# Kernel tuning notes

Hardware: AMD Instinct MI355X
Metric: run time of the kernel (lower is better)

The kernel has to match this reference:

```python
import jax, jax.numpy as jnp
import numpy as np

N_NODES = 50000


def graph_conv(src, dst, x, W, b, n_nodes):
    """DGL GraphConv, norm='both': D_out^{-1/2} A D_in^{-1/2} x W + b.
    src/dst: [E] edge endpoints (message flows src -> dst).
    """
    ones = jnp.ones(src.shape[0], dtype=x.dtype)
    deg_out = jnp.clip(jax.ops.segment_sum(ones, src, num_segments=n_nodes), 1.0)
    deg_in = jnp.clip(jax.ops.segment_sum(ones, dst, num_segments=n_nodes), 1.0)
    h = x * jax.lax.rsqrt(deg_out)[:, None]          # src-side normalization
    msgs = h[src]                                     # [E, F] gather (irregular)
    agg = jax.ops.segment_sum(msgs, dst, num_segments=n_nodes)  # SpMM scatter-add
    agg = agg * jax.lax.rsqrt(deg_in)[:, None]        # dst-side normalization
    return agg @ W + b


def setup_inputs() -> dict:
    key = jax.random.key(0)
    ks = jax.random.split(key, 9)
    E = 600000
    in_f, hid, emb = 128, 64, 32
    features = jax.random.normal(ks[0], (N_NODES, in_f), dtype=jnp.float32)
    src = jax.random.randint(ks[1], (E,), 0, N_NODES)
    dst = jax.random.randint(ks[2], (E,), 0, N_NODES)

    def glorot(k, fan_in, fan_out):
        lim = np.sqrt(6.0 / (fan_in + fan_out)).astype(np.float32)
        return jax.random.uniform(k, (fan_in, fan_out), jnp.float32, -lim, lim)

    return {
        "features": features, "src": src, "dst": dst,
        "W1": glorot(ks[3], in_f, hid), "b1": jnp.zeros((hid,), jnp.float32),
        "W2": glorot(ks[4], hid, emb), "b2": jnp.zeros((emb,), jnp.float32),
        "W3": glorot(ks[5], emb, in_f), "b3": jnp.zeros((in_f,), jnp.float32),
    }


def reference(features, src, dst, W1, b1, W2, b2, W3, b3):
    h = jax.nn.relu(graph_conv(src, dst, features, W1, b1, N_NODES))
    z = graph_conv(src, dst, h, W2, b2, N_NODES)
    recon = graph_conv(src, dst, z, W3, b3, N_NODES)
    return (z, recon)
```

## Files before the change

### kernel.cpp

```cpp
#include <hip/hip_runtime.h>
#include <hip/hip_bf16.h>


#define NN   50000
#define HPB  128
#define FNB  2
#define FBIN 25000
typedef unsigned short u16;
typedef unsigned char  u8;

__device__ __forceinline__ float bfhi(unsigned u) {
    unsigned v = u & 0xFFFF0000u;
    return __builtin_bit_cast(float, v);
}
__device__ __forceinline__ float bflo(unsigned u) {
    unsigned v = u << 16;
    return __builtin_bit_cast(float, v);
}
__device__ __forceinline__ unsigned f2bf(float f) {
    unsigned u = __builtin_bit_cast(unsigned, f);
    return (u + 0x7FFFu + ((u >> 16) & 1u)) >> 16;
}

__global__ __launch_bounds__(256) void k_hist1(
    const int* __restrict__ src, const int* __restrict__ dst,
    u8* __restrict__ slab, int E, int slice)
{
    __shared__ unsigned h[NN / 4];
    const int which = blockIdx.x / HPB;
    const int p     = blockIdx.x % HPB;
    const int* __restrict__ idx = which ? dst : src;

    for (int i = threadIdx.x; i < NN / 4; i += 256) h[i] = 0;
    __syncthreads();

    const int beg = p * slice;
    const int fin = min(beg + slice, E);
    for (int i = beg + threadIdx.x * 4; i + 3 < fin; i += 1024) {
        const int4 v = *(const int4*)(idx + i);
        atomicAdd(&h[v.x >> 2], 1u << ((v.x & 3) << 3));
        atomicAdd(&h[v.y >> 2], 1u << ((v.y & 3) << 3));
        atomicAdd(&h[v.z >> 2], 1u << ((v.z & 3) << 3));
        atomicAdd(&h[v.w >> 2], 1u << ((v.w & 3) << 3));
    }
    for (int i = beg + ((fin - beg) & ~3) + threadIdx.x; i < fin; i += 256) {
        const int u = idx[i];
        atomicAdd(&h[u >> 2], 1u << ((u & 3) << 3));
    }
    __syncthreads();

    unsigned* out = (unsigned*)(slab + (size_t)blockIdx.x * NN);
    for (int i = threadIdx.x; i < NN / 4; i += 256) out[i] = h[i];
}

__global__ __launch_bounds__(256) void k_reduce_scan(
    u8* __restrict__ slab, float* __restrict__ rs_out, float* __restrict__ rs_in,
    int* __restrict__ partial, int* __restrict__ blocksum,
    unsigned* __restrict__ csr_words, int ncw, int N)
{
    __shared__ int tmp[256];
    const int tid = threadIdx.x;
    const int i = blockIdx.x * 256 + tid;

    int run = 0;
    if (i < N) {
        const u8* s_src = slab + i;
        u8*       s_dst = slab + (size_t)HPB * NN + i;
        int so = 0;
#pragma unroll 8
        for (int p = 0; p < HPB; ++p) so += s_src[(size_t)p * NN];
#pragma unroll 8
        for (int p = 0; p < HPB; ++p) {
            const int c = s_dst[(size_t)p * NN];
            s_dst[(size_t)p * NN] = (u8)run;
            run += c;
        }
        rs_out[i] = rsqrtf(fmaxf((float)so, 1.0f));
        rs_in[i]  = rsqrtf(fmaxf((float)run, 1.0f));
    }
    const int pad = (run + 15) & ~15;
    tmp[tid] = pad; __syncthreads();
    for (int off = 1; off < 256; off <<= 1) {
        int t = (tid >= off) ? tmp[tid - off] : 0;
        __syncthreads(); tmp[tid] += t; __syncthreads();
    }
    if (i < N) partial[i] = tmp[tid];
    if (tid == 255) blocksum[blockIdx.x] = tmp[255];

    for (int w = blockIdx.x * 256 + tid; w < ncw; w += gridDim.x * 256)
        csr_words[w] = 0xC350C350u;
}

__global__ __launch_bounds__(256) void k_scan23(
    const int* __restrict__ partial, const int* __restrict__ blocksum,
    int* __restrict__ row_start, int n, int nb)
{
    __shared__ int tmp[256];
    const int tid = threadIdx.x;
    int v = (tid < nb) ? blocksum[tid] : 0;
    tmp[tid] = v; __syncthreads();
    for (int off = 1; off < 256; off <<= 1) {
        int t = (tid >= off) ? tmp[tid - off] : 0;
        __syncthreads(); tmp[tid] += t; __syncthreads();
    }
    __syncthreads();
    const int i = blockIdx.x * 256 + tid;
    if (i < n) {
        const int base = (blockIdx.x > 0) ? tmp[blockIdx.x - 1] : 0;
        row_start[i + 1] = partial[i] + base;
        if (i == 0) row_start[0] = 0;
    }
}

__global__ __launch_bounds__(256) void k_fill2(
    const int* __restrict__ src, const int* __restrict__ dst,
    const int* __restrict__ row_start, const u8* __restrict__ slab,
    u16* __restrict__ csr, int E, int slice, int N)
{
    __shared__ int cur[FBIN];
    const int bin = blockIdx.x / HPB;
    const int p   = blockIdx.x % HPB;
    const int lo  = bin * FBIN;

    const u8* part_off = slab + (size_t)(HPB + p) * NN;
    for (int j = threadIdx.x; j < FBIN; j += 256) {
        const int node = lo + j;
        cur[j] = row_start[node] + (int)part_off[node];
    }
    __syncthreads();

    const int beg = p * slice;
    const int fin = min(beg + slice, E);
    for (int i = beg + threadIdx.x * 4; i + 3 < fin; i += 1024) {
        const int4 d = *(const int4*)(dst + i);
        const int4 s = *(const int4*)(src + i);
        int u;
        u = d.x - lo; if ((unsigned)u < (unsigned)FBIN) csr[atomicAdd(&cur[u], 1)] = (u16)s.x;
        u = d.y - lo; if ((unsigned)u < (unsigned)FBIN) csr[atomicAdd(&cur[u], 1)] = (u16)s.y;
        u = d.z - lo; if ((unsigned)u < (unsigned)FBIN) csr[atomicAdd(&cur[u], 1)] = (u16)s.z;
        u = d.w - lo; if ((unsigned)u < (unsigned)FBIN) csr[atomicAdd(&cur[u], 1)] = (u16)s.w;
    }
    for (int i = beg + ((fin - beg) & ~3) + threadIdx.x; i < fin; i += 256) {
        int u = dst[i] - lo;
        if ((unsigned)u < (unsigned)FBIN) csr[atomicAdd(&cur[u], 1)] = (u16)src[i];
    }
}

template <int IN_F, int OUT_F, int TM>
__global__ __launch_bounds__(256) void k_gemm_bf16out(
    const float* __restrict__ X, const float* __restrict__ W,
    const float* __restrict__ rowscale, u16* __restrict__ Y,
    u16* __restrict__ t2b, u16* __restrict__ zb, int n)
{
    constexpr int CT  = OUT_F / 4;
    constexpr int RT  = 256 / CT;
    constexpr int RPT = TM / RT;
    constexpr int XS  = IN_F + 4;
    __shared__ float sW[IN_F * OUT_F];
    __shared__ float sX[TM * XS];
    const int tid = threadIdx.x;
    const int row0 = blockIdx.x * TM;

    if (blockIdx.x == 0) {
        if (tid < 32)      ((unsigned*)(Y   + (size_t)NN * 64))[tid]      = 0;
        else if (tid < 48) ((unsigned*)(t2b + (size_t)NN * 32))[tid - 32] = 0;
        else if (tid < 64) ((unsigned*)(zb  + (size_t)NN * 32))[tid - 48] = 0;
    }

    for (int i = tid; i < IN_F * OUT_F / 4; i += 256)
        ((float4*)sW)[i] = ((const float4*)W)[i];
    for (int i = tid; i < TM * IN_F / 4; i += 256) {
        const int r  = i / (IN_F / 4);
        const int c4 = (i % (IN_F / 4)) * 4;
        const int gr = row0 + r;
        float4 v = make_float4(0.f, 0.f, 0.f, 0.f);
        if (gr < n) v = *(const float4*)(X + (long)gr * IN_F + c4);
        *(float4*)(sX + r * XS + c4) = v;
    }
    __syncthreads();

    const int tc = tid % CT;
    const int tr = tid / CT;
    float4 acc[RPT];
#pragma unroll
    for (int i = 0; i < RPT; ++i) acc[i] = make_float4(0.f, 0.f, 0.f, 0.f);

#pragma unroll 8
    for (int k = 0; k < IN_F; ++k) {
        const float4 w = *(const float4*)(sW + k * OUT_F + 4 * tc);
#pragma unroll
        for (int i = 0; i < RPT; ++i) {
            const float xv = sX[(tr + i * RT) * XS + k];
            acc[i].x += xv * w.x; acc[i].y += xv * w.y;
            acc[i].z += xv * w.z; acc[i].w += xv * w.w;
        }
    }

#pragma unroll
    for (int i = 0; i < RPT; ++i) {
        const int gr = row0 + tr + i * RT;
        if (gr < n) {
            float4 v = acc[i];
            const float s = rowscale[gr];
            v.x *= s; v.y *= s; v.z *= s; v.w *= s;
            uint2 pk;
            pk.x = f2bf(v.x) | (f2bf(v.y) << 16);
            pk.y = f2bf(v.z) | (f2bf(v.w) << 16);
            *(uint2*)(Y + (size_t)gr * OUT_F + 4 * tc) = pk;
        }
    }
}

#define ACC8(q) do { \
    a[0] += bflo((q).x); a[1] += bfhi((q).x); a[2] += bflo((q).y); a[3] += bfhi(q.y); \
    a[4] += bflo((q).z); a[5] += bfhi((q).z); a[6] += bflo((q).w); a[7] += bfhi(q.w); } while (0)

#define GATHER4(SRCB, RW) do { \
    const uint2 w = *(const uint2*)(csr + j); \
    const int s0 = w.x & 0xFFFF, s1 = w.x >> 16; \
    const int s2 = w.y & 0xFFFF, s3 = w.y >> 16; \
    const uint4 q0 = *(const uint4*)(SRCB + (size_t)s0 * RW + c8); \
    const uint4 q1 = *(const uint4*)(SRCB + (size_t)s1 * RW + c8); \
    const uint4 q2 = *(const uint4*)(SRCB + (size_t)s2 * RW + c8); \
    const uint4 q3 = *(const uint4*)(SRCB + (size_t)s3 * RW + c8); \
    ACC8(q0); ACC8(q1); ACC8(q2); ACC8(q3); } while (0)

__global__ __launch_bounds__(256) void k_gather_gemm_B(
    const int* __restrict__ row_start, const u16* __restrict__ csr,
    const u16* __restrict__ t1b, const float* __restrict__ rs_in,
    const float* __restrict__ rs_out, const float* __restrict__ b1,
    const float* __restrict__ W2, u16* __restrict__ t2b, int N)
{
    __shared__ float sh[8][72];
    __shared__ float sW[64 * 32];
    const int tid = threadIdx.x;

    for (int i = tid; i < 64 * 32 / 4; i += 256)
        ((float4*)sW)[i] = ((const float4*)W2)[i];

    const int nloc = tid >> 5;
    const int sub  = tid & 31;
    const int qtr  = sub >> 3;
    const int c8   = (sub & 7) * 8;
    const int node = blockIdx.x * 8 + nloc;

    float a[8];
#pragma unroll
    for (int t = 0; t < 8; ++t) a[t] = 0.f;

    if (node < N) {
        const int beg  = row_start[node];
        const int qlen = (row_start[node + 1] - beg) >> 2;
        const int j0 = beg + qtr * qlen;
        const int j1 = j0 + qlen;
        for (int j = j0; j < j1; j += 4) GATHER4(t1b, 64);
    }
#pragma unroll
    for (int t = 0; t < 8; ++t) {
        a[t] += __shfl_xor(a[t], 8);
        a[t] += __shfl_xor(a[t], 16);
    }

    if (node < N && qtr == 0) {
        const float rs = rs_in[node];
#pragma unroll
        for (int t = 0; t < 8; ++t)
            sh[nloc][c8 + t] = fmaxf(a[t] * rs + b1[c8 + t], 0.f);
    }
    __syncthreads();

    if (tid < 64) {
        const int n2 = tid >> 3;
        const int c4 = (tid & 7) * 4;
        float4 acc = make_float4(0.f, 0.f, 0.f, 0.f);
#pragma unroll 8
        for (int k = 0; k < 64; ++k) {
            const float xv = sh[n2][k];
            const float4 w = *(const float4*)(sW + k * 32 + c4);
            acc.x += xv * w.x; acc.y += xv * w.y; acc.z += xv * w.z; acc.w += xv * w.w;
        }
        const int gn = blockIdx.x * 8 + n2;
        if (gn < N) {
            const float s = rs_out[gn];
            uint2 pk;
            pk.x = f2bf(acc.x * s) | (f2bf(acc.y * s) << 16);
            pk.y = f2bf(acc.z * s) | (f2bf(acc.w * s) << 16);
            *(uint2*)(t2b + (size_t)gn * 32 + c4) = pk;
        }
    }
}

__global__ __launch_bounds__(256) void k_gather_C(
    const int* __restrict__ row_start, const u16* __restrict__ csr,
    const u16* __restrict__ t2b, const float* __restrict__ rs_in,
    const float* __restrict__ rs_out, const float* __restrict__ b2,
    float* __restrict__ z, u16* __restrict__ zb, int N)
{
    const int node = blockIdx.x * 16 + (threadIdx.x >> 4);
    const int sub  = threadIdx.x & 15;
    const int qtr  = sub >> 2;
    const int c8   = (sub & 3) * 8;
    if (node >= N) return;

    const int beg  = row_start[node];
    const int qlen = (row_start[node + 1] - beg) >> 2;
    const int j0 = beg + qtr * qlen;
    const int j1 = j0 + qlen;

    float a[8];
#pragma unroll
    for (int t = 0; t < 8; ++t) a[t] = 0.f;
    for (int j = j0; j < j1; j += 4) GATHER4(t2b, 32);

#pragma unroll
    for (int t = 0; t < 8; ++t) {
        a[t] += __shfl_xor(a[t], 4);
        a[t] += __shfl_xor(a[t], 8);
    }
    if (qtr) return;

    const float rs = rs_in[node];
    float v[8];
#pragma unroll
    for (int t = 0; t < 8; ++t) v[t] = a[t] * rs + b2[c8 + t];

    float* o = z + (size_t)node * 32 + c8;
    *(float4*)(o)     = make_float4(v[0], v[1], v[2], v[3]);
    *(float4*)(o + 4) = make_float4(v[4], v[5], v[6], v[7]);

    const float ss = rs_out[node];
    uint4 pk;
    pk.x = f2bf(v[0] * ss) | (f2bf(v[1] * ss) << 16);
    pk.y = f2bf(v[2] * ss) | (f2bf(v[3] * ss) << 16);
    pk.z = f2bf(v[4] * ss) | (f2bf(v[5] * ss) << 16);
    pk.w = f2bf(v[6] * ss) | (f2bf(v[7] * ss) << 16);
    *(uint4*)(zb + (size_t)node * 32 + c8) = pk;
}

__global__ __launch_bounds__(256) void k_gather_gemm_D(
    const int* __restrict__ row_start, const u16* __restrict__ csr,
    const u16* __restrict__ zb, const float* __restrict__ rs_in,
    const float* __restrict__ W3, const float* __restrict__ b3,
    float* __restrict__ recon, int N)
{
    __shared__ float sa[16][36];
    __shared__ float sW[32 * 128];
    const int tid = threadIdx.x;

    for (int i = tid; i < 32 * 128 / 4; i += 256)
        ((float4*)sW)[i] = ((const float4*)W3)[i];

    const int nloc = tid >> 4;
    const int sub  = tid & 15;
    const int qtr  = sub >> 2;
    const int c8   = (sub & 3) * 8;
    const int node = blockIdx.x * 16 + nloc;

    float a[8];
#pragma unroll
    for (int t = 0; t < 8; ++t) a[t] = 0.f;

    if (node < N) {
        const int beg  = row_start[node];
        const int qlen = (row_start[node + 1] - beg) >> 2;
        const int j0 = beg + qtr * qlen;
        const int j1 = j0 + qlen;
        for (int j = j0; j < j1; j += 4) GATHER4(zb, 32);
    }
#pragma unroll
    for (int t = 0; t < 8; ++t) {
        a[t] += __shfl_xor(a[t], 4);
        a[t] += __shfl_xor(a[t], 8);
    }

    if (node < N && qtr == 0) {
        const float rs = rs_in[node];
#pragma unroll
        for (int t = 0; t < 8; ++t) sa[nloc][c8 + t] = a[t] * rs;
    }
    __syncthreads();

    const int ng = (tid >> 5) * 2;
    const int c4 = (tid & 31) * 4;
    const float4 bb = *(const float4*)(b3 + c4);
    float4 acc[2];
    acc[0] = bb; acc[1] = bb;
#pragma unroll 4
    for (int k = 0; k < 32; ++k) {
        const float4 w = *(const float4*)(sW + k * 128 + c4);
#pragma unroll
        for (int i = 0; i < 2; ++i) {
            const float xv = sa[ng + i][k];
            acc[i].x += xv * w.x; acc[i].y += xv * w.y;
            acc[i].z += xv * w.z; acc[i].w += xv * w.w;
        }
    }
#pragma unroll
    for (int i = 0; i < 2; ++i) {
        const int gn = blockIdx.x * 16 + ng + i;
        if (gn < N) *(float4*)(recon + (size_t)gn * 128 + c4) = acc[i];
    }
}

extern "C" void kernel_launch(void* const* d_in, const int* in_sizes, int n_in,
                              void* d_out, int out_size, void* d_ws, size_t ws_size,
                              hipStream_t stream) {
    const float* feat = (const float*)d_in[0];
    const int*   src  = (const int*)d_in[1];
    const int*   dst  = (const int*)d_in[2];
    const float* W1   = (const float*)d_in[3];
    const float* b1   = (const float*)d_in[4];
    const float* W2   = (const float*)d_in[5];
    const float* b2   = (const float*)d_in[6];
    const float* W3   = (const float*)d_in[7];
    const float* b3   = (const float*)d_in[8];

    const int E = in_sizes[1];
    const int N = in_sizes[0] / 128;
    const int slice = (((E + HPB - 1) / HPB) + 3) & ~3;
    const int CSRMAX = E + 15 * N;
    const int ncw = CSRMAX / 2;

    const size_t SLABB = 2UL * HPB * NN;
    u8*  slab     = (u8*)d_ws;
    int* row_start= (int*)(slab + SLABB);
    int* scan_p   = row_start + N + 16;
    int* blocksum = scan_p + N;
    u16* csr      = (u16*)(blocksum + 256);
    float* rs_out = (float*)(csr + CSRMAX);
    float* rs_in  = rs_out + N;
    u16* t2b      = (u16*)(rs_in + N);
    u16* zb       = t2b + (size_t)(N + 8) * 32;
    u16* t1b      = (u16*)slab;

    float* z_out  = (float*)d_out;
    float* recon  = z_out + (size_t)N * 32;

    const int B = 256;
    const int nb_scan = (N + 255) / 256;

    k_hist1<<<2 * HPB, B, 0, stream>>>(src, dst, slab, E, slice);
    k_reduce_scan<<<nb_scan, B, 0, stream>>>(slab, rs_out, rs_in, scan_p, blocksum,
                                             (unsigned*)csr, ncw, N);
    k_scan23<<<nb_scan, B, 0, stream>>>(scan_p, blocksum, row_start, N, nb_scan);
    k_fill2<<<FNB * HPB, B, 0, stream>>>(src, dst, row_start, slab, csr, E, slice, N);

    k_gemm_bf16out<128, 64, 32><<<(N + 31) / 32, B, 0, stream>>>(
        feat, W1, rs_out, t1b, t2b, zb, N);

    k_gather_gemm_B<<<(N + 7) / 8, B, 0, stream>>>(
        row_start, csr, t1b, rs_in, rs_out, b1, W2, t2b, N);

    k_gather_C<<<(N + 15) / 16, B, 0, stream>>>(
        row_start, csr, t2b, rs_in, rs_out, b2, z_out, zb, N);

    k_gather_gemm_D<<<(N + 15) / 16, B, 0, stream>>>(
        row_start, csr, zb, rs_in, W3, b3, recon, N);
}
```

Before: 190.9 us.

## Use MFMA bf16 for first GEMM, shrink src histogram, batch more nodes per block

Replaces the scalar fp32 first-layer GEMM with a bf16 MFMA 16x16x32 kernel that converts X and W1 to bf16 in shared memory. Cuts the source-degree histogram from 128 to 32 blocks, since only its total count is needed. The layer-2 and layer-3 gather+GEMM kernels now process 32 nodes per block, reusing the staged weights over more rows and making fewer weight loads. Rounding the inputs to bf16 before the matmul adds precision error, and the MFMA output is written with scalar 16-bit stores.

After: 185.9 us. 1.03x faster.

```diff
diff --git a/kernel.cpp b/kernel.cpp
--- a/kernel.cpp
+++ b/kernel.cpp
@@ -3,11 +3,14 @@
 
 
 #define NN   50000
-#define HPB  128
+#define HPS  32
+#define HPD  128
 #define FNB  2
 #define FBIN 25000
 typedef unsigned short u16;
 typedef unsigned char  u8;
+typedef __attribute__((ext_vector_type(8))) short bf16x8;
+typedef __attribute__((ext_vector_type(4))) float f32x4;
 
 __device__ __forceinline__ float bfhi(unsigned u) {
     unsigned v = u & 0xFFFF0000u;
@@ -24,12 +27,13 @@
 
 __global__ __launch_bounds__(256) void k_hist1(
     const int* __restrict__ src, const int* __restrict__ dst,
-    u8* __restrict__ slab, int E, int slice)
+    u8* __restrict__ slab, int E, int slice_s, int slice_d)
 {
     __shared__ unsigned h[NN / 4];
-    const int which = blockIdx.x / HPB;
-    const int p     = blockIdx.x % HPB;
-    const int* __restrict__ idx = which ? dst : src;
+    const bool is_src = blockIdx.x < HPS;
+    const int p       = is_src ? blockIdx.x : blockIdx.x - HPS;
+    const int slice   = is_src ? slice_s : slice_d;
+    const int* __restrict__ idx = is_src ? src : dst;
 
     for (int i = threadIdx.x; i < NN / 4; i += 256) h[i] = 0;
     __syncthreads();
@@ -65,12 +69,12 @@
     int run = 0;
     if (i < N) {
         const u8* s_src = slab + i;
-        u8*       s_dst = slab + (size_t)HPB * NN + i;
+        u8*       s_dst = slab + (size_t)HPS * NN + i;
         int so = 0;
 #pragma unroll 8
-        for (int p = 0; p < HPB; ++p) so += s_src[(size_t)p * NN];
+        for (int p = 0; p < HPS; ++p) so += s_src[(size_t)p * NN];
 #pragma unroll 8
-        for (int p = 0; p < HPB; ++p) {
+        for (int p = 0; p < HPD; ++p) {
             const int c = s_dst[(size_t)p * NN];
             s_dst[(size_t)p * NN] = (u8)run;
             run += c;
@@ -118,11 +122,11 @@
     u16* __restrict__ csr, int E, int slice, int N)
 {
     __shared__ int cur[FBIN];
-    const int bin = blockIdx.x / HPB;
-    const int p   = blockIdx.x % HPB;
+    const int bin = blockIdx.x / HPD;
+    const int p   = blockIdx.x % HPD;
     const int lo  = bin * FBIN;
 
-    const u8* part_off = slab + (size_t)(HPB + p) * NN;
+    const u8* part_off = slab + (size_t)(HPS + p) * NN;
     for (int j = threadIdx.x; j < FBIN; j += 256) {
         const int node = lo + j;
         cur[j] = row_start[node] + (int)part_off[node];
@@ -146,20 +150,16 @@
     }
 }
 
-template <int IN_F, int OUT_F, int TM>
-__global__ __launch_bounds__(256) void k_gemm_bf16out(
-    const float* __restrict__ X, const float* __restrict__ W,
-    const float* __restrict__ rowscale, u16* __restrict__ Y,
-    u16* __restrict__ t2b, u16* __restrict__ zb, int n)
-{
-    constexpr int CT  = OUT_F / 4;
-    constexpr int RT  = 256 / CT;
-    constexpr int RPT = TM / RT;
-    constexpr int XS  = IN_F + 4;
-    __shared__ float sW[IN_F * OUT_F];
-    __shared__ float sX[TM * XS];
+#define XS1 136
+__global__ __launch_bounds__(256) void k_gemm_mfma_A(
+    const float* __restrict__ X, const float* __restrict__ W1,
+    const float* __restrict__ rs, u16* __restrict__ Y,
+    u16* __restrict__ t2b, u16* __restrict__ zb, int N)
+{
+    __shared__ u16 sXb[64 * XS1];
+    __shared__ u16 sWt[64 * XS1];
     const int tid = threadIdx.x;
-    const int row0 = blockIdx.x * TM;
+    const int m0 = blockIdx.x * 64;
 
     if (blockIdx.x == 0) {
         if (tid < 32)      ((unsigned*)(Y   + (size_t)NN * 64))[tid]      = 0;
@@ -167,53 +167,59 @@
         else if (tid < 64) ((unsigned*)(zb  + (size_t)NN * 32))[tid - 48] = 0;
     }
 
-    for (int i = tid; i < IN_F * OUT_F / 4; i += 256)
-        ((float4*)sW)[i] = ((const float4*)W)[i];
-    for (int i = tid; i < TM * IN_F / 4; i += 256) {
-        const int r  = i / (IN_F / 4);
-        const int c4 = (i % (IN_F / 4)) * 4;
-        const int gr = row0 + r;
+    for (int i = tid; i < 128 * 64; i += 256) {
+        const int k = i >> 6, n = i & 63;
+        sWt[n * XS1 + k] = (u16)f2bf(W1[i]);
+    }
+    for (int i = tid; i < 64 * 32; i += 256) {
+        const int r  = i >> 5;
+        const int c4 = (i & 31) * 4;
+        const int gr = m0 + r;
         float4 v = make_float4(0.f, 0.f, 0.f, 0.f);
-        if (gr < n) v = *(const float4*)(X + (long)gr * IN_F + c4);
-        *(float4*)(sX + r * XS + c4) = v;
-    }
-    __syncthreads();
-
-    const int tc = tid % CT;
-    const int tr = tid / CT;
-    float4 acc[RPT];
-#pragma unroll
-    for (int i = 0; i < RPT; ++i) acc[i] = make_float4(0.f, 0.f, 0.f, 0.f);
-
-#pragma unroll 8
-    for (int k = 0; k < IN_F; ++k) {
-        const float4 w = *(const float4*)(sW + k * OUT_F + 4 * tc);
-#pragma unroll
-        for (int i = 0; i < RPT; ++i) {
-            const float xv = sX[(tr + i * RT) * XS + k];
-            acc[i].x += xv * w.x; acc[i].y += xv * w.y;
-            acc[i].z += xv * w.z; acc[i].w += xv * w.w;
-        }
-    }
-
-#pragma unroll
-    for (int i = 0; i < RPT; ++i) {
-        const int gr = row0 + tr + i * RT;
-        if (gr < n) {
-            float4 v = acc[i];
-            const float s = rowscale[gr];
-            v.x *= s; v.y *= s; v.z *= s; v.w *= s;
-            uint2 pk;
-            pk.x = f2bf(v.x) | (f2bf(v.y) << 16);
-            pk.y = f2bf(v.z) | (f2bf(v.w) << 16);
-            *(uint2*)(Y + (size_t)gr * OUT_F + 4 * tc) = pk;
+        if (gr < N) v = *(const float4*)(X + (size_t)gr * 128 + c4);
+        uint2 pk;
+        pk.x = f2bf(v.x) | (f2bf(v.y) << 16);
+        pk.y = f2bf(v.z) | (f2bf(v.w) << 16);
+        *(uint2*)(sXb + r * XS1 + c4) = pk;
+    }
+    __syncthreads();
+
+    const int wv   = tid >> 6;
+    const int lane = tid & 63;
+    const int l15  = lane & 15;
+    const int quad = lane >> 4;
+
+    f32x4 acc[4] = {};
+    const u16* ax = sXb + (wv * 16 + l15) * XS1 + quad * 8;
+    const u16* bx = sWt + l15 * XS1 + quad * 8;
+#pragma unroll
+    for (int ks = 0; ks < 4; ++ks) {
+        const bf16x8 af = *(const bf16x8*)(ax + ks * 32);
+#pragma unroll
+        for (int nt = 0; nt < 4; ++nt) {
+            const bf16x8 bf = *(const bf16x8*)(bx + nt * 16 * XS1 + ks * 32);
+            acc[nt] = __builtin_amdgcn_mfma_f32_16x16x32_bf16(af, bf, acc[nt], 0, 0, 0);
+        }
+    }
+
+    const int mrow = m0 + wv * 16 + quad * 4;
+    float sc[4];
+#pragma unroll
+    for (int r = 0; r < 4; ++r) sc[r] = (mrow + r < N) ? rs[mrow + r] : 0.f;
+#pragma unroll
+    for (int r = 0; r < 4; ++r) {
+        const int gr = mrow + r;
+        if (gr < N) {
+#pragma unroll
+            for (int nt = 0; nt < 4; ++nt)
+                Y[(size_t)gr * 64 + nt * 16 + l15] = (u16)f2bf(acc[nt][r] * sc[r]);
         }
     }
 }
 
 #define ACC8(q) do { \
-    a[0] += bflo((q).x); a[1] += bfhi((q).x); a[2] += bflo((q).y); a[3] += bfhi(q.y); \
-    a[4] += bflo((q).z); a[5] += bfhi((q).z); a[6] += bflo((q).w); a[7] += bfhi(q.w); } while (0)
+    a[0] += bflo((q).x); a[1] += bfhi((q).x); a[2] += bflo((q).y); a[3] += bfhi((q).y); \
+    a[4] += bflo((q).z); a[5] += bfhi((q).z); a[6] += bflo((q).w); a[7] += bfhi((q).w); } while (0)
 
 #define GATHER4(SRCB, RW) do { \
     const uint2 w = *(const uint2*)(csr + j); \
@@ -231,62 +237,62 @@
     const float* __restrict__ rs_out, const float* __restrict__ b1,
     const float* __restrict__ W2, u16* __restrict__ t2b, int N)
 {
-    __shared__ float sh[8][72];
+    __shared__ float sh[32][72];
     __shared__ float sW[64 * 32];
     const int tid = threadIdx.x;
 
     for (int i = tid; i < 64 * 32 / 4; i += 256)
         ((float4*)sW)[i] = ((const float4*)W2)[i];
 
-    const int nloc = tid >> 5;
+    const int nb   = tid >> 5;
     const int sub  = tid & 31;
     const int qtr  = sub >> 3;
     const int c8   = (sub & 7) * 8;
-    const int node = blockIdx.x * 8 + nloc;
-
-    float a[8];
-#pragma unroll
-    for (int t = 0; t < 8; ++t) a[t] = 0.f;
-
-    if (node < N) {
-        const int beg  = row_start[node];
-        const int qlen = (row_start[node + 1] - beg) >> 2;
-        const int j0 = beg + qtr * qlen;
-        const int j1 = j0 + qlen;
-        for (int j = j0; j < j1; j += 4) GATHER4(t1b, 64);
-    }
-#pragma unroll
-    for (int t = 0; t < 8; ++t) {
-        a[t] += __shfl_xor(a[t], 8);
-        a[t] += __shfl_xor(a[t], 16);
-    }
-
-    if (node < N && qtr == 0) {
-        const float rs = rs_in[node];
-#pragma unroll
-        for (int t = 0; t < 8; ++t)
-            sh[nloc][c8 + t] = fmaxf(a[t] * rs + b1[c8 + t], 0.f);
-    }
-    __syncthreads();
-
-    if (tid < 64) {
-        const int n2 = tid >> 3;
-        const int c4 = (tid & 7) * 4;
-        float4 acc = make_float4(0.f, 0.f, 0.f, 0.f);
+
+#pragma unroll
+    for (int b = 0; b < 4; ++b) {
+        const int nloc = b * 8 + nb;
+        const int node = blockIdx.x * 32 + nloc;
+        float a[8];
+#pragma unroll
+        for (int t = 0; t < 8; ++t) a[t] = 0.f;
+        if (node < N) {
+            const int beg  = row_start[node];
+            const int qlen = (row_start[node + 1] - beg) >> 2;
+            const int j0 = beg + qtr * qlen;
+            const int j1 = j0 + qlen;
+            for (int j = j0; j < j1; j += 4) GATHER4(t1b, 64);
+        }
+#pragma unroll
+        for (int t = 0; t < 8; ++t) {
+            a[t] += __shfl_xor(a[t], 8);
+            a[t] += __shfl_xor(a[t], 16);
+        }
+        if (node < N && qtr == 0) {
+            const float rs = rs_in[node];
+#pragma unroll
+            for (int t = 0; t < 8; ++t)
+                sh[nloc][c8 + t] = fmaxf(a[t] * rs + b1[c8 + t], 0.f);
+        }
+    }
+    __syncthreads();
+
+    const int n2 = tid >> 3;
+    const int c4 = (tid & 7) * 4;
+    float4 acc = make_float4(0.f, 0.f, 0.f, 0.f);
 #pragma unroll 8
-        for (int k = 0; k < 64; ++k) {
-            const float xv = sh[n2][k];
-            const float4 w = *(const float4*)(sW + k * 32 + c4);
-            acc.x += xv * w.x; acc.y += xv * w.y; acc.z += xv * w.z; acc.w += xv * w.w;
-        }
-        const int gn = blockIdx.x * 8 + n2;
-        if (gn < N) {
-            const float s = rs_out[gn];
-            uint2 pk;
-            pk.x = f2bf(acc.x * s) | (f2bf(acc.y * s) << 16);
-            pk.y = f2bf(acc.z * s) | (f2bf(acc.w * s) << 16);
-            *(uint2*)(t2b + (size_t)gn * 32 + c4) = pk;
-        }
+    for (int k = 0; k < 64; ++k) {
+        const float xv = sh[n2][k];
+        const float4 w = *(const float4*)(sW + k * 32 + c4);
+        acc.x += xv * w.x; acc.y += xv * w.y; acc.z += xv * w.z; acc.w += xv * w.w;
+    }
+    const int gn = blockIdx.x * 32 + n2;
+    if (gn < N) {
+        const float s = rs_out[gn];
+        uint2 pk;
+        pk.x = f2bf(acc.x * s) | (f2bf(acc.y * s) << 16);
+        pk.y = f2bf(acc.z * s) | (f2bf(acc.w * s) << 16);
+        *(uint2*)(t2b + (size_t)gn * 32 + c4) = pk;
     }
 }
 
@@ -343,61 +349,64 @@
     const float* __restrict__ W3, const float* __restrict__ b3,
     float* __restrict__ recon, int N)
 {
-    __shared__ float sa[16][36];
+    __shared__ float sa[32][36];
     __shared__ float sW[32 * 128];
     const int tid = threadIdx.x;
 
     for (int i = tid; i < 32 * 128 / 4; i += 256)
         ((float4*)sW)[i] = ((const float4*)W3)[i];
 
-    const int nloc = tid >> 4;
+    const int nb   = tid >> 4;
     const int sub  = tid & 15;
     const int qtr  = sub >> 2;
     const int c8   = (sub & 3) * 8;
-    const int node = blockIdx.x * 16 + nloc;
-
-    float a[8];
-#pragma unroll
-    for (int t = 0; t < 8; ++t) a[t] = 0.f;
-
-    if (node < N) {
-        const int beg  = row_start[node];
-        const int qlen = (row_start[node + 1] - beg) >> 2;
-        const int j0 = beg + qtr * qlen;
-        const int j1 = j0 + qlen;
-        for (int j = j0; j < j1; j += 4) GATHER4(zb, 32);
-    }
-#pragma unroll
-    for (int t = 0; t < 8; ++t) {
-        a[t] += __shfl_xor(a[t], 4);
-        a[t] += __shfl_xor(a[t], 8);
-    }
-
-    if (node < N && qtr == 0) {
-        const float rs = rs_in[node];
-#pragma unroll
-        for (int t = 0; t < 8; ++t) sa[nloc][c8 + t] = a[t] * rs;
-    }
-    __syncthreads();
-
-    const int ng = (tid >> 5) * 2;
+
+#pragma unroll
+    for (int b = 0; b < 2; ++b) {
+        const int nloc = b * 16 + nb;
+        const int node = blockIdx.x * 32 + nloc;
+        float a[8];
+#pragma unroll
+        for (int t = 0; t < 8; ++t) a[t] = 0.f;
+        if (node < N) {
+            const int beg  = row_start[node];
+            const int qlen = (row_start[node + 1] - beg) >> 2;
+            const int j0 = beg + qtr * qlen;
+            const int j1 = j0 + qlen;
+            for (int j = j0; j < j1; j += 4) GATHER4(zb, 32);
+        }
+#pragma unroll
+        for (int t = 0; t < 8; ++t) {
+            a[t] += __shfl_xor(a[t], 4);
+            a[t] += __shfl_xor(a[t], 8);
+        }
+        if (node < N && qtr == 0) {
+            const float rs = rs_in[node];
+#pragma unroll
+            for (int t = 0; t < 8; ++t) sa[nloc][c8 + t] = a[t] * rs;
+        }
+    }
+    __syncthreads();
+
+    const int ng = (tid >> 5) * 4;
     const int c4 = (tid & 31) * 4;
     const float4 bb = *(const float4*)(b3 + c4);
-    float4 acc[2];
-    acc[0] = bb; acc[1] = bb;
+    float4 acc[4];
+#pragma unroll
+    for (int i = 0; i < 4; ++i) acc[i] = bb;
 #pragma unroll 4
     for (int k = 0; k < 32; ++k) {
         const float4 w = *(const float4*)(sW + k * 128 + c4);
 #pragma unroll
-        for (int i = 0; i < 2; ++i) {
+        for (int i = 0; i < 4; ++i) {
             const float xv = sa[ng + i][k];
             acc[i].x += xv * w.x; acc[i].y += xv * w.y;
             acc[i].z += xv * w.z; acc[i].w += xv * w.w;
         }
     }
 #pragma unroll
-    for (int i = 0; i < 2; ++i) {
-        const int gn = blockIdx.x * 16 + ng + i;
+    for (int i = 0; i < 4; ++i) {
+        const int gn = blockIdx.x * 32 + ng + i;
         if (gn < N) *(float4*)(recon + (size_t)gn * 128 + c4) = acc[i];
     }
 }
@@ -417,11 +426,12 @@
 
     const int E = in_sizes[1];
     const int N = in_sizes[0] / 128;
-    const int slice = (((E + HPB - 1) / HPB) + 3) & ~3;
+    const int slice_s = (((E + HPS - 1) / HPS) + 3) & ~3;
+    const int slice_d = (((E + HPD - 1) / HPD) + 3) & ~3;
     const int CSRMAX = E + 15 * N;
     const int ncw = CSRMAX / 2;
 
-    const size_t SLABB = 2UL * HPB * NN;
+    const size_t SLABB = (size_t)(HPS + HPD) * NN;
     u8*  slab     = (u8*)d_ws;
     int* row_start= (int*)(slab + SLABB);
     int* scan_p   = row_start + N + 16;
@@ -439,21 +449,21 @@
     const int B = 256;
     const int nb_scan = (N + 255) / 256;
 
-    k_hist1<<<2 * HPB, B, 0, stream>>>(src, dst, slab, E, slice);
+    k_hist1<<<HPS + HPD, B, 0, stream>>>(src, dst, slab, E, slice_s, slice_d);
     k_reduce_scan<<<nb_scan, B, 0, stream>>>(slab, rs_out, rs_in, scan_p, blocksum,
                                              (unsigned*)csr, ncw, N);
     k_scan23<<<nb_scan, B, 0, stream>>>(scan_p, blocksum, row_start, N, nb_scan);
-    k_fill2<<<FNB * HPB, B, 0, stream>>>(src, dst, row_start, slab, csr, E, slice, N);
-
-    k_gemm_bf16out<128, 64, 32><<<(N + 31) / 32, B, 0, stream>>>(
+    k_fill2<<<FNB * HPD, B, 0, stream>>>(src, dst, row_start, slab, csr, E, slice_d, N);
+
+    k_gemm_mfma_A<<<(N + 63) / 64, B, 0, stream>>>(
         feat, W1, rs_out, t1b, t2b, zb, N);
 
-    k_gather_gemm_B<<<(N + 7) / 8, B, 0, stream>>>(
+    k_gather_gemm_B<<<(N + 31) / 32, B, 0, stream>>>(
         row_start, csr, t1b, rs_in, rs_out, b1, W2, t2b, N);
 
     k_gather_C<<<(N + 15) / 16, B, 0, stream>>>(
         row_start, csr, t2b, rs_in, rs_out, b2, z_out, zb, N);
 
-    k_gather_gemm_D<<<(N + 15) / 16, B, 0, stream>>>(
+    k_gather_gemm_D<<<(N + 31) / 32, B, 0, stream>>>(
         row_start, csr, zb, rs_in, W3, b3, recon, N);
 }
```
